# Kernel tuning notes

Hardware: AMD Instinct MI355X
Metric: run time of the kernel (lower is better)

## Reference

```python
import jax, jax.numpy as jnp
import numpy as np

D_MODEL = 1024
N_HEAD = 16
HEAD_DIM = D_MODEL // N_HEAD
D_FF = 4096
N_EXPERTS = 4
EPS = 1e-05


def _layer_norm(x, gamma, beta):
    mu = jnp.mean(x, axis=-1, keepdims=True)
    var = jnp.mean((x - mu) ** 2, axis=-1, keepdims=True)
    return (x - mu) / jnp.sqrt(var + EPS) * gamma + beta


def setup_inputs() -> dict:
    key = jax.random.key(0)
    ks = jax.random.split(key, 20)
    f32 = jnp.float32
    sc = 1.0 / np.sqrt(D_MODEL)
    scf = 1.0 / np.sqrt(D_FF)
    return {
        "src": jax.random.normal(ks[0], (4, 512, D_MODEL), f32),
        "Wq": jax.random.normal(ks[1], (D_MODEL, D_MODEL), f32) * sc,
        "bq": jnp.zeros((D_MODEL,), f32),
        "Wk": jax.random.normal(ks[2], (D_MODEL, D_MODEL), f32) * sc,
        "bk": jnp.zeros((D_MODEL,), f32),
        "Wv": jax.random.normal(ks[3], (D_MODEL, D_MODEL), f32) * sc,
        "bv": jnp.zeros((D_MODEL,), f32),
        "Wo": jax.random.normal(ks[4], (D_MODEL, D_MODEL), f32) * sc,
        "bo": jnp.zeros((D_MODEL,), f32),
        "router_w": jax.random.normal(ks[5], (D_MODEL, 1), f32) * 0.05,
        "router_b": jnp.zeros((1,), f32),
        "W1": jax.random.normal(ks[6], (N_EXPERTS, D_MODEL, D_FF), f32) * sc,
        "b1": jnp.zeros((N_EXPERTS, D_FF), f32),
        "W2": jax.random.normal(ks[7], (N_EXPERTS, D_FF, D_MODEL), f32) * scf,
        "b2": jnp.zeros((N_EXPERTS, D_MODEL), f32),
        "ln1_g": jnp.ones((D_MODEL,), f32),
        "ln1_b": jnp.zeros((D_MODEL,), f32),
        "ln2_g": jnp.ones((D_MODEL,), f32),
        "ln2_b": jnp.zeros((D_MODEL,), f32),
    }


def reference(src, Wq, bq, Wk, bk, Wv, bv, Wo, bo, router_w, router_b,
              W1, b1, W2, b2, ln1_g, ln1_b, ln2_g, ln2_b):
    B, T, _ = src.shape
    # --- self attention ---
    q = (src @ Wq + bq).reshape(B, T, N_HEAD, HEAD_DIM)
    k = (src @ Wk + bk).reshape(B, T, N_HEAD, HEAD_DIM)
    v = (src @ Wv + bv).reshape(B, T, N_HEAD, HEAD_DIM)
    scale = HEAD_DIM ** -0.5
    scores = jnp.einsum('bqhd,bkhd->bhqk', q, k) * scale
    probs = jax.nn.softmax(scores, axis=-1)
    attn = jnp.einsum('bhqk,bkhd->bqhd', probs, v).reshape(B, T, D_MODEL)
    attn = attn @ Wo + bo
    x = _layer_norm(src + attn, ln1_g, ln1_b)
    # --- hash-routed single-expert MoE FFN ---
    keys = (x @ router_w + router_b)[..., 0]           # [B, T]
    expert_idx = jnp.remainder(jnp.floor(keys).astype(jnp.int32), N_EXPERTS)
    ff_out = jnp.zeros_like(x)
    for e in range(N_EXPERTS):
        h = jax.nn.relu(x @ W1[e] + b1[e])             # [B, T, D_FF]
        y = h @ W2[e] + b2[e]                          # [B, T, D_MODEL]
        ff_out = ff_out + jnp.where((expert_idx == e)[..., None], y, 0.0)
    return _layer_norm(x + ff_out, ln2_g, ln2_b)
```

## Files before the change

kernel.cpp:

```cpp
#include <hip/hip_runtime.h>
#include <hip/hip_bf16.h>
#include <stdint.h>

typedef unsigned short u16;
typedef __attribute__((ext_vector_type(8))) short s8v;
typedef __attribute__((ext_vector_type(4))) float f4v;

#define DEVI static __device__ __forceinline__

DEVI u16 f2bf(float x) {
  union { float f; unsigned u; } a; a.f = x;
  return (u16)((a.u + 0x7fffu + ((a.u >> 16) & 1u)) >> 16);
}
DEVI float bf2f(u16 h) {
  union { float f; unsigned u; } a; a.u = ((unsigned)h) << 16; return a.f;
}
DEVI float wred_add(float s) {
#pragma unroll
  for (int o = 32; o; o >>= 1) s += __shfl_xor(s, o, 64);
  return s;
}
DEVI float wred_max(float s) {
#pragma unroll
  for (int o = 32; o; o >>= 1) s = fmaxf(s, __shfl_xor(s, o, 64));
  return s;
}
DEVI f4v mfma16(s8v a, s8v b, f4v c) {
  return __builtin_amdgcn_mfma_f32_16x16x32_bf16(a, b, c, 0, 0, 0);
}

DEVI int rho(int j) { return ((j & 12) << 1) | (j & 3) | ((j >> 4) << 2); }

DEVI void gload16(const u16* gp, u16* lp) {
  __builtin_amdgcn_global_load_lds(
      (const __attribute__((address_space(1))) uint32_t*)gp,
      (__attribute__((address_space(3))) uint32_t*)lp, 16, 0, 0);
}

DEVI s8v ldfrag_sw(const u16* base, int r, int lg) {
  int off = ((r >> 4) << 9) + ((r & 15) << 5) + ((lg ^ ((r >> 1) & 3)) << 3);
  return *(const s8v*)(base + off);
}

__global__ __launch_bounds__(256) void split_k(const float* __restrict__ in,
                                               u16* __restrict__ h, u16* __restrict__ l, int n4) {
  int i = blockIdx.x * 256 + threadIdx.x;
  if (i >= n4) return;
  float4 v = ((const float4*)in)[i];
  ushort4 hv, lv;
  hv.x = f2bf(v.x); lv.x = f2bf(v.x - bf2f(hv.x));
  hv.y = f2bf(v.y); lv.y = f2bf(v.y - bf2f(hv.y));
  hv.z = f2bf(v.z); lv.z = f2bf(v.z - bf2f(hv.z));
  hv.w = f2bf(v.w); lv.w = f2bf(v.w - bf2f(hv.w));
  int t = i & 7, blk = i >> 3;
  int si = blk * 8 + ((t & 3) << 1) + (t >> 2);
  ((ushort4*)h)[si] = hv;
  ((ushort4*)l)[si] = lv;
}

template<bool LO>
__global__ __launch_bounds__(256) void transpose_split_k(const float* __restrict__ in, long long zIn,
                                                         u16* __restrict__ outH, u16* __restrict__ outL,
                                                         long long zOut, int R, int C) {
  __shared__ float t[32][33];
  in += (long long)blockIdx.z * zIn;
  outH += (long long)blockIdx.z * zOut;
  if (LO) outL += (long long)blockIdx.z * zOut;
  const int cc = blockIdx.x * 32, rr = blockIdx.y * 32;
  const int tx = threadIdx.x, ty = threadIdx.y;
#pragma unroll
  for (int i = 0; i < 4; ++i)
    t[ty * 4 + i][tx] = in[(long long)(rr + ty * 4 + i) * C + cc + tx];
  __syncthreads();
  const int rtx = rho(tx);
#pragma unroll
  for (int i = 0; i < 4; ++i) {
    float v = t[tx][ty * 4 + i];
    long long o = (long long)(cc + ty * 4 + i) * R + rr + rtx;
    u16 h = f2bf(v);
    outH[o] = h;
    if (LO) outL[o] = f2bf(v - bf2f(h));
  }
}

__global__ __launch_bounds__(256) void transpose_pair_k(const u16* __restrict__ inH, const u16* __restrict__ inL,
                                                        u16* __restrict__ oH, u16* __restrict__ oL) {
  __shared__ u16 th[32][34], tl[32][34];
  const int b = blockIdx.z;
  const int dd = blockIdx.x * 32;
  const int tt = blockIdx.y * 32;
  const int tx = threadIdx.x, ty = threadIdx.y;
  const int64_t ibase = ((int64_t)(b * 512 + tt)) * 3072 + 2048 + dd;
  const int rtx = rho(tx);
#pragma unroll
  for (int i = 0; i < 4; ++i) {
    int rr = ty * 4 + i;
    th[rr][tx] = inH[ibase + (int64_t)rr * 3072 + rtx];
    tl[rr][tx] = inL[ibase + (int64_t)rr * 3072 + rtx];
  }
  __syncthreads();
  const int64_t obase = ((int64_t)b * 1024 + dd) * 512 + tt;
#pragma unroll
  for (int i = 0; i < 4; ++i) {
    int rr = ty * 4 + i;
    oH[obase + (int64_t)rr * 512 + rtx] = th[tx][rr];
    oL[obase + (int64_t)rr * 512 + rtx] = tl[tx][rr];
  }
}

__global__ __launch_bounds__(256) void catb_k(const float* __restrict__ a, const float* __restrict__ b,
                                              const float* __restrict__ c, float* __restrict__ o) {
  int i = blockIdx.x * 256 + threadIdx.x;
  if (i >= 3072) return;
  o[i] = i < 1024 ? a[i] : (i < 2048 ? b[i - 1024] : c[i - 2048]);
}

struct GemmArgs {
  const u16* Ah; const u16* Al; int lda;
  const u16* Bh; const u16* Bl; int ldb;
  float* C; u16* Ch; u16* Cl; int ldc;
  const float* bias;
  int K;
  int Z2;
  int64_t aZ1, aZ2, bZ1, bZ2, cZ1, cZ2;
  const int* ofs;
  int64_t bStrE; int biasStrE;
};

template<int BM, int BN, bool SPLIT, int EPI, bool PN>
__global__ __launch_bounds__(256) void gemm_k(GemmArgs g) {
  constexpr int ASZ = BM * 32, BSZ = BN * 32;
  constexpr int AN = SPLIT ? 2 * ASZ : ASZ;
  constexpr int BNT = SPLIT ? 2 * BSZ : BSZ;
  constexpr int NLOAD = (BM / 64 + BN / 64) * (SPLIT ? 2 : 1);
  __shared__ __align__(16) u16 sA[2][AN];
  __shared__ __align__(16) u16 sB[2][BNT];

  const int tid = threadIdx.x;
  const u16* Ah = g.Ah; const u16* Al = g.Al;
  const u16* Bh = g.Bh; const u16* Bl = g.Bl;
  int64_t cOff = 0;
  if (g.Z2 > 0) {
    int z1 = blockIdx.z / g.Z2, z2 = blockIdx.z % g.Z2;
    int64_t ao = (int64_t)z1 * g.aZ1 + (int64_t)z2 * g.aZ2;
    int64_t bo = (int64_t)z1 * g.bZ1 + (int64_t)z2 * g.bZ2;
    Ah += ao; Bh += bo;
    if (SPLIT) { Al += ao; Bl += bo; }
    cOff = (int64_t)z1 * g.cZ1 + (int64_t)z2 * g.cZ2;
  }
  const int row0 = blockIdx.x * BM;
  const int col0 = blockIdx.y * BN;
  const float* bias = g.bias;
  if (g.ofs) {
    if (row0 >= g.ofs[4]) return;
    int e = 0;
    while (e < 3 && row0 >= g.ofs[e + 1]) ++e;
    Bh += (int64_t)e * g.bStrE;
    if (bias) bias += (int64_t)e * g.biasStrE;
  }

  const int w = tid >> 6, lane = tid & 63;
  const int wr = w >> 1, wc = w & 1;
  const int lr = lane & 15, lg = lane >> 4;
  constexpr int FM = BM / 32, FN = BN / 32;

  const int srow = lane >> 2;
  const int sG = (lane & 3) ^ ((lane >> 3) & 3);

  auto stage = [&](int b, int kt) {
#pragma unroll
    for (int c = 0; c < BM / 64; ++c) {
      int ch = c * 4 + w;
      int64_t go = (int64_t)(row0 + ch * 16 + srow) * g.lda + kt + sG * 8;
      gload16(Ah + go, &sA[b][ch * 512]);
      if (SPLIT) gload16(Al + go, &sA[b][ASZ + ch * 512]);
    }
#pragma unroll
    for (int c = 0; c < BN / 64; ++c) {
      int ch = c * 4 + w;
      int64_t go = (int64_t)(col0 + ch * 16 + srow) * g.ldb + kt + sG * 8;
      gload16(Bh + go, &sB[b][ch * 512]);
      if (SPLIT) gload16(Bl + go, &sB[b][BSZ + ch * 512]);
    }
  };

  f4v acc[FM][FN];
#pragma unroll
  for (int i = 0; i < FM; ++i)
#pragma unroll
    for (int j = 0; j < FN; ++j) acc[i][j] = f4v{0.f, 0.f, 0.f, 0.f};

  stage(0, 0);
  stage(1, 32);
  asm volatile("s_waitcnt vmcnt(%0)" :: "n"(NLOAD) : "memory");
  __builtin_amdgcn_sched_barrier(0);
  __builtin_amdgcn_s_barrier();

  const int nt = g.K >> 5;
  for (int t = 0; t < nt; ++t) {
    const int cur = t & 1;
    s8v af[FM], bfr[FN], afl[SPLIT ? FM : 1], bfl[SPLIT ? FN : 1];
#pragma unroll
    for (int mi = 0; mi < FM; ++mi) {
      int r = wr * (BM / 2) + mi * 16 + lr;
      af[mi] = ldfrag_sw(&sA[cur][0], r, lg);
      if (SPLIT) afl[mi] = ldfrag_sw(&sA[cur][ASZ], r, lg);
    }
#pragma unroll
    for (int ni = 0; ni < FN; ++ni) {
      int r = wc * (BN / 2) + ni * 16 + lr;
      bfr[ni] = ldfrag_sw(&sB[cur][0], r, lg);
      if (SPLIT) bfl[ni] = ldfrag_sw(&sB[cur][BSZ], r, lg);
    }
    asm volatile("s_waitcnt lgkmcnt(0)" ::: "memory");
    __builtin_amdgcn_sched_barrier(0);
    __builtin_amdgcn_s_barrier();
    if (t + 2 < nt) stage(cur, (t + 2) << 5);
    __builtin_amdgcn_s_setprio(1);
#pragma unroll
    for (int mi = 0; mi < FM; ++mi)
#pragma unroll
      for (int ni = 0; ni < FN; ++ni) {
        acc[mi][ni] = mfma16(af[mi], bfr[ni], acc[mi][ni]);
        if (SPLIT) {
          acc[mi][ni] = mfma16(af[mi], bfl[ni], acc[mi][ni]);
          acc[mi][ni] = mfma16(afl[mi], bfr[ni], acc[mi][ni]);
        }
      }
    __builtin_amdgcn_s_setprio(0);
    if (t + 1 < nt) {
      if (t + 2 < nt)
        asm volatile("s_waitcnt vmcnt(%0)" :: "n"(NLOAD) : "memory");
      else
        asm volatile("s_waitcnt vmcnt(0)" ::: "memory");
      __builtin_amdgcn_sched_barrier(0);
      __builtin_amdgcn_s_barrier();
    }
  }
#pragma unroll
  for (int mi = 0; mi < FM; ++mi) {
    int rbase = row0 + wr * (BM / 2) + mi * 16 + lg * 4;
#pragma unroll
    for (int ni = 0; ni < FN; ++ni) {
      int c = col0 + wc * (BN / 2) + ni * 16 + lr;
      int cs = c;
      if (PN) {
        int jr = ((lr >> 2) << 3) | (lr & 3) | ((ni & 1) << 2);
        cs = (c & ~31) | jr;
      }
      float bv = bias ? bias[c] : 0.f;
#pragma unroll
      for (int j = 0; j < 4; ++j) {
        int r = rbase + j;
        float v = acc[mi][ni][j] + bv;
        if (EPI == 0) {
          g.C[cOff + (int64_t)r * g.ldc + cs] = v;
        } else if (EPI == 1) {
          u16 h = f2bf(v);
          int64_t o = cOff + (int64_t)r * g.ldc + cs;
          g.Ch[o] = h;
          g.Cl[o] = f2bf(v - bf2f(h));
        } else {
          v = v > 0.f ? v : 0.f;
          g.Ch[cOff + (int64_t)r * g.ldc + cs] = f2bf(v);
        }
      }
    }
  }
}

__global__ __launch_bounds__(256) void reduce_k(const float* __restrict__ part, const int* __restrict__ rowsrc,
                                                const int* __restrict__ ofs, const float* __restrict__ b2,
                                                float* __restrict__ y) {
  int r = blockIdx.x;
  if (r >= ofs[4]) return;
  int s = rowsrc[r];
  if (s < 0) return;
  int e = 0;
  while (e < 3 && r >= ofs[e + 1]) ++e;
  int c = threadIdx.x;
  const int64_t RN = 2560ll * 1024;
  float4 v0 = ((const float4*)(part + 0 * RN + (int64_t)r * 1024))[c];
  float4 v1 = ((const float4*)(part + 1 * RN + (int64_t)r * 1024))[c];
  float4 bb = ((const float4*)(b2 + (int64_t)e * 1024))[c];
  float4 o;
  o.x = (v0.x + v1.x) + bb.x;
  o.y = (v0.y + v1.y) + bb.y;
  o.z = (v0.z + v1.z) + bb.z;
  o.w = (v0.w + v1.w) + bb.w;
  ((float4*)(y + (int64_t)s * 1024))[c] = o;
}

__global__ __launch_bounds__(128) void softmax_k(float* __restrict__ scores) {
  __shared__ float sm[2];
  const int64_t row = blockIdx.x;
  float* p = scores + row * 512;
  const int tid = threadIdx.x, w = tid >> 6, lane = tid & 63;
  float4 v = ((const float4*)p)[tid];
  v.x *= 0.125f; v.y *= 0.125f; v.z *= 0.125f; v.w *= 0.125f;
  float m = wred_max(fmaxf(fmaxf(v.x, v.y), fmaxf(v.z, v.w)));
  if (lane == 0) sm[w] = m;
  __syncthreads();
  m = fmaxf(sm[0], sm[1]);
  float e0 = expf(v.x - m), e1 = expf(v.y - m), e2 = expf(v.z - m), e3 = expf(v.w - m);
  float s = wred_add(e0 + e1 + e2 + e3);
  __syncthreads();
  if (lane == 0) sm[w] = s;
  __syncthreads();
  float inv = 1.f / (sm[0] + sm[1]);
  e0 *= inv; e1 *= inv; e2 *= inv; e3 *= inv;
  u16* ph = (u16*)p;
  ushort4 hv, lv;
  hv.x = f2bf(e0); lv.x = f2bf(e0 - bf2f(hv.x));
  hv.y = f2bf(e1); lv.y = f2bf(e1 - bf2f(hv.y));
  hv.z = f2bf(e2); lv.z = f2bf(e2 - bf2f(hv.z));
  hv.w = f2bf(e3); lv.w = f2bf(e3 - bf2f(hv.w));
  ((ushort4*)ph)[tid] = hv;
  ((ushort4*)(ph + 512))[tid] = lv;
}

__global__ __launch_bounds__(256) void ln_k(const float* __restrict__ a, const float* __restrict__ b,
                                            const float* __restrict__ gm, const float* __restrict__ bt,
                                            float* __restrict__ out) {
  __shared__ float sm[4];
  const int r = blockIdx.x, tid = threadIdx.x;
  const int w = tid >> 6, lane = tid & 63;
  float4 va = ((const float4*)(a + (int64_t)r * 1024))[tid];
  float4 vb = ((const float4*)(b + (int64_t)r * 1024))[tid];
  float x0 = va.x + vb.x, x1 = va.y + vb.y, x2 = va.z + vb.z, x3 = va.w + vb.w;
  float s = wred_add(x0 + x1 + x2 + x3);
  if (lane == 0) sm[w] = s;
  __syncthreads();
  float mu = (sm[0] + sm[1] + sm[2] + sm[3]) * (1.f / 1024.f);
  float d0 = x0 - mu, d1 = x1 - mu, d2 = x2 - mu, d3 = x3 - mu;
  float q = wred_add(d0 * d0 + d1 * d1 + d2 * d2 + d3 * d3);
  __syncthreads();
  if (lane == 0) sm[w] = q;
  __syncthreads();
  float var = (sm[0] + sm[1] + sm[2] + sm[3]) * (1.f / 1024.f);
  float rs = 1.f / sqrtf(var + 1e-5f);
  float4 g4 = ((const float4*)gm)[tid];
  float4 b4 = ((const float4*)bt)[tid];
  float4 o;
  o.x = d0 * rs * g4.x + b4.x;
  o.y = d1 * rs * g4.y + b4.y;
  o.z = d2 * rs * g4.z + b4.z;
  o.w = d3 * rs * g4.w + b4.w;
  ((float4*)(out + (int64_t)r * 1024))[tid] = o;
}

__global__ __launch_bounds__(256) void router_k(const float* __restrict__ x, const float* __restrict__ rw,
                                                const float* __restrict__ rb, int* __restrict__ eidx) {
  int t = blockIdx.x * 4 + (threadIdx.x >> 6);
  int lane = threadIdx.x & 63;
  const float* xr = x + (int64_t)t * 1024;
  float s = 0.f;
#pragma unroll
  for (int i = 0; i < 16; ++i) {
    int c = i * 64 + lane;
    s += xr[c] * rw[c];
  }
  s = wred_add(s);
  if (lane == 0) {
    float key = s + rb[0];
    int f = (int)floorf(key);
    eidx[t] = f & 3;
  }
}

__global__ __launch_bounds__(256) void compact_k(const int* __restrict__ eidx,
                                                 int* __restrict__ rowsrc, int* __restrict__ ofs) {
  __shared__ unsigned long long sc[256];
  __shared__ int soff[5];
  const int tid = threadIdx.x;
  int myE[8];
  unsigned long long c = 0;
#pragma unroll
  for (int i = 0; i < 8; ++i) {
    int e = eidx[tid * 8 + i];
    myE[i] = e;
    c += 1ull << (e * 16);
  }
  sc[tid] = c;
  __syncthreads();
  for (int o = 1; o < 256; o <<= 1) {
    unsigned long long v = (tid >= o) ? sc[tid - o] : 0ull;
    __syncthreads();
    sc[tid] += v;
    __syncthreads();
  }
  unsigned long long incl = sc[tid], tot = sc[255];
  unsigned long long excl = incl - c;
  if (tid == 0) {
    int off = 0;
    for (int e = 0; e < 4; ++e) {
      soff[e] = off;
      int cnt = (int)((tot >> (e * 16)) & 0xffff);
      off += (cnt + 127) & ~127;
    }
    soff[4] = off;
    for (int e = 0; e < 5; ++e) ofs[e] = soff[e];
  }
  __syncthreads();
  for (int r = tid; r < 2560; r += 256) rowsrc[r] = -1;
  __threadfence_block();
  __syncthreads();
  int rank[4];
#pragma unroll
  for (int e = 0; e < 4; ++e) rank[e] = (int)((excl >> (e * 16)) & 0xffff);
#pragma unroll
  for (int i = 0; i < 8; ++i) {
    int e = myE[i];
    rowsrc[soff[e] + rank[e]] = tid * 8 + i;
    rank[e]++;
  }
}

__global__ __launch_bounds__(256) void gather_k(const float* __restrict__ x, const int* __restrict__ rowsrc,
                                                const int* __restrict__ ofs, u16* __restrict__ xg) {
  int r = blockIdx.x;
  if (r >= ofs[4]) return;
  int s = rowsrc[r];
  int c = threadIdx.x;
  float4 v = (s >= 0) ? ((const float4*)(x + (int64_t)s * 1024))[c] : float4{0.f, 0.f, 0.f, 0.f};
  ushort4 o;
  o.x = f2bf(v.x); o.y = f2bf(v.y); o.z = f2bf(v.z); o.w = f2bf(v.w);
  int t = c & 7, blk = c >> 3;
  int si = blk * 8 + ((t & 3) << 1) + (t >> 2);
  ((ushort4*)(xg + (int64_t)r * 1024))[si] = o;
}

extern "C" void kernel_launch(void* const* d_in, const int* in_sizes, int n_in,
                              void* d_out, int out_size, void* d_ws, size_t ws_size,
                              hipStream_t stream) {
  const float* src = (const float*)d_in[0];
  const float* Wq  = (const float*)d_in[1];
  const float* bq  = (const float*)d_in[2];
  const float* Wk  = (const float*)d_in[3];
  const float* bk  = (const float*)d_in[4];
  const float* Wv  = (const float*)d_in[5];
  const float* bv  = (const float*)d_in[6];
  const float* Wo  = (const float*)d_in[7];
  const float* bo  = (const float*)d_in[8];
  const float* rw  = (const float*)d_in[9];
  const float* rb  = (const float*)d_in[10];
  const float* W1  = (const float*)d_in[11];
  const float* b1  = (const float*)d_in[12];
  const float* W2  = (const float*)d_in[13];
  const float* b2  = (const float*)d_in[14];
  const float* g1  = (const float*)d_in[15];
  const float* be1 = (const float*)d_in[16];
  const float* g2  = (const float*)d_in[17];
  const float* be2 = (const float*)d_in[18];
  float* out = (float*)d_out;

  char* base = (char*)d_ws;
  size_t off = 0;
  auto alloc = [&](size_t bytes) -> char* {
    char* p = base + off;
    off += (bytes + 255) & ~(size_t)255;
    return p;
  };
  const size_t MB = 1ull << 20;
  u16* srcH = (u16*)alloc(4 * MB);
  u16* srcL = (u16*)alloc(4 * MB);
  u16* WqkvTh = (u16*)alloc(6 * MB);
  u16* WqkvTl = (u16*)alloc(6 * MB);
  u16* WoTh = (u16*)alloc(2 * MB);
  u16* WoTl = (u16*)alloc(2 * MB);
  float* bqkv = (float*)alloc(16 * 1024);
  u16* qkvH = (u16*)alloc(12 * MB);
  u16* qkvL = (u16*)alloc(12 * MB);
  u16* hbuf = (u16*)qkvH;
  u16* vTH = (u16*)alloc(4 * MB); u16* vTL = (u16*)alloc(4 * MB);
  float* scores = (float*)alloc(64 * MB);
  u16* W1T = (u16*)scores;
  u16* W2T = (u16*)scores + 16ull * 1024 * 1024;
  u16* attnH = (u16*)alloc(4 * MB); u16* attnL = (u16*)alloc(4 * MB);
  u16* xg = (u16*)attnH;
  float* woOut = (float*)alloc(8 * MB);
  float* ybuf = (float*)woOut;
  float* xbuf = (float*)alloc(8 * MB);
  float* partials = (float*)alloc(20 * MB);
  int* eidx   = (int*)alloc(2048 * 4);
  int* rowsrc = (int*)alloc(2560 * 4);
  int* ofs    = (int*)alloc(32);
  (void)ws_size; (void)in_sizes; (void)n_in; (void)out_size;

  dim3 tb(32, 8);

  split_k<<<2048, 256, 0, stream>>>(src, srcH, srcL, 2048 * 1024 / 4);
  transpose_split_k<true><<<dim3(32, 32, 1), tb, 0, stream>>>(Wq, 0, WqkvTh, WqkvTl, 0, 1024, 1024);
  transpose_split_k<true><<<dim3(32, 32, 1), tb, 0, stream>>>(Wk, 0, WqkvTh + 1024 * 1024, WqkvTl + 1024 * 1024, 0, 1024, 1024);
  transpose_split_k<true><<<dim3(32, 32, 1), tb, 0, stream>>>(Wv, 0, WqkvTh + 2 * 1024 * 1024, WqkvTl + 2 * 1024 * 1024, 0, 1024, 1024);
  transpose_split_k<true><<<dim3(32, 32, 1), tb, 0, stream>>>(Wo, 0, WoTh, WoTl, 0, 1024, 1024);
  catb_k<<<12, 256, 0, stream>>>(bq, bk, bv, bqkv);

  {
    GemmArgs g{};
    g.Ah = srcH; g.Al = srcL; g.lda = 1024;
    g.Bh = WqkvTh; g.Bl = WqkvTl; g.ldb = 1024;
    g.Ch = qkvH; g.Cl = qkvL; g.ldc = 3072;
    g.bias = bqkv; g.K = 1024; g.Z2 = 0;
    gemm_k<128, 128, true, 1, true><<<dim3(16, 24, 1), 256, 0, stream>>>(g);
  }
  transpose_pair_k<<<dim3(32, 16, 4), tb, 0, stream>>>(qkvH, qkvL, vTH, vTL);

  {
    GemmArgs g{};
    g.Ah = qkvH; g.Al = qkvL; g.lda = 3072;
    g.Bh = qkvH + 1024; g.Bl = qkvL + 1024; g.ldb = 3072;
    g.C = scores; g.ldc = 512;
    g.K = 64; g.Z2 = 16;
    g.aZ1 = 512ll * 3072; g.aZ2 = 64;
    g.bZ1 = 512ll * 3072; g.bZ2 = 64;
    g.cZ1 = 16ll * 512 * 512; g.cZ2 = 512ll * 512;
    gemm_k<128, 64, true, 0, true><<<dim3(4, 8, 64), 256, 0, stream>>>(g);
  }
  softmax_k<<<64 * 512, 128, 0, stream>>>(scores);
  {
    GemmArgs g{};
    g.Ah = (const u16*)scores; g.Al = (const u16*)scores + 512; g.lda = 1024;
    g.Bh = vTH; g.Bl = vTL; g.ldb = 512;
    g.Ch = attnH; g.Cl = attnL; g.ldc = 1024;
    g.K = 512; g.Z2 = 16;
    g.aZ1 = 16ll * 512 * 1024; g.aZ2 = 512ll * 1024;
    g.bZ1 = 1024ll * 512;      g.bZ2 = 64ll * 512;
    g.cZ1 = 512ll * 1024;      g.cZ2 = 64;
    gemm_k<64, 64, true, 1, true><<<dim3(8, 1, 64), 256, 0, stream>>>(g);
  }
  {
    GemmArgs g{};
    g.Ah = attnH; g.Al = attnL; g.lda = 1024;
    g.Bh = WoTh; g.Bl = WoTl; g.ldb = 1024;
    g.C = woOut; g.ldc = 1024;
    g.bias = bo; g.K = 1024; g.Z2 = 0;
    gemm_k<64, 64, true, 0, false><<<dim3(32, 16, 1), 256, 0, stream>>>(g);
  }
  ln_k<<<2048, 256, 0, stream>>>(src, woOut, g1, be1, xbuf);

  router_k<<<512, 256, 0, stream>>>(xbuf, rw, rb, eidx);
  compact_k<<<1, 256, 0, stream>>>(eidx, rowsrc, ofs);
  gather_k<<<2560, 256, 0, stream>>>(xbuf, rowsrc, ofs, xg);

  transpose_split_k<false><<<dim3(128, 32, 4), tb, 0, stream>>>(W1, 1024ll * 4096, W1T, nullptr, 4096ll * 1024, 1024, 4096);
  transpose_split_k<false><<<dim3(32, 128, 4), tb, 0, stream>>>(W2, 4096ll * 1024, W2T, nullptr, 1024ll * 4096, 4096, 1024);

  {
    GemmArgs g{};
    g.Ah = xg; g.lda = 1024;
    g.Bh = W1T; g.ldb = 1024;
    g.Ch = hbuf; g.ldc = 4096;
    g.bias = b1; g.biasStrE = 4096;
    g.K = 1024; g.Z2 = 0;
    g.ofs = ofs; g.bStrE = 4096ll * 1024;
    gemm_k<128, 128, false, 2, true><<<dim3(20, 32, 1), 256, 0, stream>>>(g);
  }
  {
    GemmArgs g{};
    g.Ah = hbuf; g.lda = 4096;
    g.Bh = W2T; g.ldb = 4096;
    g.C = partials; g.ldc = 1024;
    g.bias = nullptr;
    g.K = 2048; g.Z2 = 2;
    g.aZ1 = 0; g.aZ2 = 2048;
    g.bZ1 = 0; g.bZ2 = 2048;
    g.cZ1 = 0; g.cZ2 = 2560ll * 1024;
    g.ofs = ofs; g.bStrE = 4096ll * 1024;
    gemm_k<128, 64, false, 0, false><<<dim3(20, 16, 2), 256, 0, stream>>>(g);
  }
  reduce_k<<<2560, 256, 0, stream>>>(partials, rowsrc, ofs, b2, ybuf);
  ln_k<<<2048, 256, 0, stream>>>(xbuf, ybuf, g2, be2, out);
}
```

Measured before the change: 312.0 us.

## Double-buffer GEMM LDS fragments in registers and retile the QKV projection

The GEMM main loop is restructured to keep two register sets of A/B fragments. The next K-tile's fragments are read from shared memory before the current tile's MFMAs are issued, so LDS reads can overlap matrix math. The loop is unrolled by two to swap the register buffers, and launch_bounds now asks for 3 blocks per CU. The QKV projection also moves from 128x128 to 128x64 tiles, doubling the grid. The cost is higher register pressure from the duplicated fragments, and correctness now assumes the K-tile count is even.

```diff
diff --git a/kernel.cpp b/kernel.cpp
--- a/kernel.cpp
+++ b/kernel.cpp
@@ -128,7 +128,7 @@
 };
 
 template<int BM, int BN, bool SPLIT, int EPI, bool PN>
-__global__ __launch_bounds__(256) void gemm_k(GemmArgs g) {
+__global__ __launch_bounds__(256, 3) void gemm_k(GemmArgs g) {
   constexpr int ASZ = BM * 32, BSZ = BN * 32;
   constexpr int AN = SPLIT ? 2 * ASZ : ASZ;
   constexpr int BNT = SPLIT ? 2 * BSZ : BSZ;
@@ -190,44 +190,39 @@
 #pragma unroll
     for (int j = 0; j < FN; ++j) acc[i][j] = f4v{0.f, 0.f, 0.f, 0.f};
 
+  s8v a0[FM], b0[FN], al0[SPLIT ? FM : 1], bl0[SPLIT ? FN : 1];
+  s8v a1[FM], b1[FN], al1[SPLIT ? FM : 1], bl1[SPLIT ? FN : 1];
+
+  auto rdfrags = [&](int buf, auto& af, auto& bf, auto& afl, auto& bfl) {
+#pragma unroll
+    for (int mi = 0; mi < FM; ++mi) {
+      int r = wr * (BM / 2) + mi * 16 + lr;
+      af[mi] = ldfrag_sw(&sA[buf][0], r, lg);
+      if (SPLIT) afl[mi] = ldfrag_sw(&sA[buf][ASZ], r, lg);
+    }
+#pragma unroll
+    for (int ni = 0; ni < FN; ++ni) {
+      int r = wc * (BN / 2) + ni * 16 + lr;
+      bf[ni] = ldfrag_sw(&sB[buf][0], r, lg);
+      if (SPLIT) bfl[ni] = ldfrag_sw(&sB[buf][BSZ], r, lg);
+    }
+  };
+
+  const int nt = g.K >> 5;
+
   stage(0, 0);
   stage(1, 32);
   asm volatile("s_waitcnt vmcnt(%0)" :: "n"(NLOAD) : "memory");
   __builtin_amdgcn_sched_barrier(0);
   __builtin_amdgcn_s_barrier();
-
-  const int nt = g.K >> 5;
-  for (int t = 0; t < nt; ++t) {
-    const int cur = t & 1;
-    s8v af[FM], bfr[FN], afl[SPLIT ? FM : 1], bfl[SPLIT ? FN : 1];
-#pragma unroll
-    for (int mi = 0; mi < FM; ++mi) {
-      int r = wr * (BM / 2) + mi * 16 + lr;
-      af[mi] = ldfrag_sw(&sA[cur][0], r, lg);
-      if (SPLIT) afl[mi] = ldfrag_sw(&sA[cur][ASZ], r, lg);
-    }
-#pragma unroll
-    for (int ni = 0; ni < FN; ++ni) {
-      int r = wc * (BN / 2) + ni * 16 + lr;
-      bfr[ni] = ldfrag_sw(&sB[cur][0], r, lg);
-      if (SPLIT) bfl[ni] = ldfrag_sw(&sB[cur][BSZ], r, lg);
-    }
+  rdfrags(0, a0, b0, al0, bl0);
+
+  auto body = [&](int t, auto& cA, auto& cB, auto& cAl, auto& cBl,
+                  auto& nA, auto& nB, auto& nAl, auto& nBl) {
     asm volatile("s_waitcnt lgkmcnt(0)" ::: "memory");
     __builtin_amdgcn_sched_barrier(0);
     __builtin_amdgcn_s_barrier();
-    if (t + 2 < nt) stage(cur, (t + 2) << 5);
-    __builtin_amdgcn_s_setprio(1);
-#pragma unroll
-    for (int mi = 0; mi < FM; ++mi)
-#pragma unroll
-      for (int ni = 0; ni < FN; ++ni) {
-        acc[mi][ni] = mfma16(af[mi], bfr[ni], acc[mi][ni]);
-        if (SPLIT) {
-          acc[mi][ni] = mfma16(af[mi], bfl[ni], acc[mi][ni]);
-          acc[mi][ni] = mfma16(afl[mi], bfr[ni], acc[mi][ni]);
-        }
-      }
-    __builtin_amdgcn_s_setprio(0);
+    if (t + 2 < nt) stage(t & 1, (t + 2) << 5);
     if (t + 1 < nt) {
       if (t + 2 < nt)
         asm volatile("s_waitcnt vmcnt(%0)" :: "n"(NLOAD) : "memory");
@@ -235,8 +230,27 @@
         asm volatile("s_waitcnt vmcnt(0)" ::: "memory");
       __builtin_amdgcn_sched_barrier(0);
       __builtin_amdgcn_s_barrier();
-    }
-  }
+      rdfrags((t + 1) & 1, nA, nB, nAl, nBl);
+    }
+    __builtin_amdgcn_s_setprio(1);
+#pragma unroll
+    for (int mi = 0; mi < FM; ++mi)
+#pragma unroll
+      for (int ni = 0; ni < FN; ++ni) {
+        acc[mi][ni] = mfma16(cA[mi], cB[ni], acc[mi][ni]);
+        if (SPLIT) {
+          acc[mi][ni] = mfma16(cA[mi], cBl[ni], acc[mi][ni]);
+          acc[mi][ni] = mfma16(cAl[mi], cB[ni], acc[mi][ni]);
+        }
+      }
+    __builtin_amdgcn_s_setprio(0);
+  };
+
+  for (int t = 0; t < nt; t += 2) {
+    body(t,     a0, b0, al0, bl0, a1, b1, al1, bl1);
+    body(t + 1, a1, b1, al1, bl1, a0, b0, al0, bl0);
+  }
+
 #pragma unroll
   for (int mi = 0; mi < FM; ++mi) {
     int rbase = row0 + wr * (BM / 2) + mi * 16 + lg * 4;
@@ -502,7 +516,7 @@
     g.Bh = WqkvTh; g.Bl = WqkvTl; g.ldb = 1024;
     g.Ch = qkvH; g.Cl = qkvL; g.ldc = 3072;
     g.bias = bqkv; g.K = 1024; g.Z2 = 0;
-    gemm_k<128, 128, true, 1, true><<<dim3(16, 24, 1), 256, 0, stream>>>(g);
+    gemm_k<128, 64, true, 1, true><<<dim3(16, 48, 1), 256, 0, stream>>>(g);
   }
   transpose_pair_k<<<dim3(32, 16, 4), tb, 0, stream>>>(qkvH, qkvL, vTH, vTL);
 
```

New measurement: 316.4 us. No clear change (+1.4%).
